# Optimization experiments

Measured on AMD Instinct MI355X. Metric: run time of the kernel, lower is better.

## Reference

```python
import jax, jax.numpy as jnp
import numpy as np

B, N, K, NUM_CLASSES = 8, 4096, 16, 40
M = B * N


def _safe_norm(v):
    s = jnp.sum(v * v, axis=-1)
    return jnp.where(s > 0, jnp.sqrt(jnp.where(s > 0, s, 1.0)), 0.0)


def _angle(v1, v2):
    cn = _safe_norm(jnp.cross(v1, v2))
    d = jnp.sum(v1 * v2, axis=-1)
    ok = (cn > 0) | (d != 0)
    return jnp.where(ok, jnp.arctan2(cn, jnp.where(ok, d, 1.0)), 0.0)


def _ppf(pos_i, pos_j, n_i, n_j):
    # PyG point_pair_features: pseudo = pos_j - pos_i (j = source, i = target)
    pseudo = pos_j - pos_i
    return jnp.stack([_safe_norm(pseudo), _angle(n_i, pseudo),
                      _angle(n_j, pseudo), _angle(n_i, n_j)], axis=-1)


def _knn_edges(pos):
    # knn_graph(k=K, loop=False), per-graph; returns (src, dst) with self-loops
    # appended (PPFConv add_self_loops=True default).
    p = pos.reshape(B, N, 3)
    sq = jnp.sum(p * p, axis=-1)                                   # [B,N]
    d2 = sq[:, :, None] + sq[:, None, :] - 2.0 * jnp.einsum('bnd,bmd->bnm', p, p)
    d2 = jnp.where(jnp.eye(N, dtype=bool)[None], jnp.inf, d2)      # no loops
    _, nbr = jax.lax.top_k(-d2, K)                                  # [B,N,K]
    offs = (jnp.arange(B) * N)[:, None, None]
    src = (nbr + offs).reshape(-1)                                  # neighbors j
    dst = jnp.repeat(jnp.arange(M), K)                              # targets i
    loops = jnp.arange(M)
    return jnp.concatenate([src, loops]), jnp.concatenate([dst, loops])


def _mlp(e, w1, b1, w2, b2):
    return jax.nn.relu(e @ w1 + b1) @ w2 + b2


def setup_inputs() -> dict:
    key = jax.random.key(0)
    ks = jax.random.split(key, 12)
    pos = jax.random.normal(ks[0], (M, 3), jnp.float32)
    nrm = jax.random.normal(ks[1], (M, 3), jnp.float32)
    nrm = nrm / jnp.linalg.norm(nrm, axis=-1, keepdims=True)
    batch = jnp.repeat(jnp.arange(B, dtype=jnp.int32), N)
    s = 0.1
    return {
        'pos': pos, 'normal': nrm, 'batch': batch,
        'w1a': jax.random.normal(ks[2], (4, 32)) * s,  'b1a': jnp.zeros(32),
        'w1b': jax.random.normal(ks[3], (32, 32)) * s, 'b1b': jnp.zeros(32),
        'w2a': jax.random.normal(ks[4], (36, 32)) * s, 'b2a': jnp.zeros(32),
        'w2b': jax.random.normal(ks[5], (32, 32)) * s, 'b2b': jnp.zeros(32),
        'wc':  jax.random.normal(ks[6], (32, NUM_CLASSES)) * s,
        'bc':  jnp.zeros(NUM_CLASSES),
    }


def reference(pos, normal, batch, w1a, b1a, w1b, b1b, w2a, b2a, w2b, b2b, wc, bc):
    src, dst = _knn_edges(pos)
    feats = _ppf(pos[dst], pos[src], normal[dst], normal[src])      # [E,4]
    # conv1: x=None -> message = mlp1(ppf), scatter-max per target node
    msg1 = _mlp(feats, w1a, b1a, w1b, b1b)
    x = jax.nn.relu(jax.ops.segment_max(msg1, dst, num_segments=M))  # [M,32]
    # conv2: message = mlp2([x_j, ppf])
    msg2 = _mlp(jnp.concatenate([x[src], feats], axis=-1), w2a, b2a, w2b, b2b)
    x = jax.nn.relu(jax.ops.segment_max(msg2, dst, num_segments=M))
    # global_max_pool over each graph (uniform batch: reshape)
    g = x.reshape(B, N, 32).max(axis=1)                              # [B,32]
    return g @ wc + bc                                               # [B,40]
```

## Files before the change

kernel.cpp:

```cpp
#include <hip/hip_runtime.h>
#include <hip/hip_bf16.h>
#include <math.h>

#define NB 8
#define NN 4096
#define KK 16
#define MM (NB*NN)
#define CH 32
#define SLOTS 17
#define NCLS 40
#define BIG 3.0e38f
#define CAP 96
#define NPB 32
#define NBLK (MM/NPB)
#define HROW 36
#define HALF 2048

#define OW1A 0
#define OB1A 128
#define OW1B 160
#define OB1B 1184
#define OW2A 1216
#define OB2A 2368
#define OW2B 2400
#define OB2B 3424
#define OWC  3456
#define OBC  4736
#define NWTS 4776

typedef short short8 __attribute__((ext_vector_type(8)));
typedef float f32x4  __attribute__((ext_vector_type(4)));
typedef float f32x2  __attribute__((ext_vector_type(2)));

__device__ float4 g_pos4[MM];
__device__ float4 g_nrm4[MM];
__device__ int    g_nbr[MM*KK];
__device__ float  g_u[MM*CH];
__device__ float  g_bmax[NBLK*CH];
__device__ float  g_wts[NWTS];
__device__ __align__(16) float4 g_fe4[MM*SLOTS];
__device__ __align__(16) unsigned short g_wfrag1[2][2][64][8];
__device__ __align__(16) unsigned short g_wfrag2[2][2][64][8];

__device__ __forceinline__ float bf(const __hip_bfloat16 x) { return __bfloat162float(x); }

__device__ __forceinline__ float ldf(const void* p, int i, bool f32) {
  return f32 ? ((const float*)p)[i] : bf(((const __hip_bfloat16*)p)[i]);
}

__device__ __forceinline__ float angf(float ax, float ay, float az,
                                      float bx, float by, float bz) {
  float cx = ay*bz - az*by;
  float cy = az*bx - ax*bz;
  float cz = ax*by - ay*bx;
  float s  = cx*cx + cy*cy + cz*cz;
  float cn = s > 0.f ? sqrtf(s) : 0.f;
  float d  = ax*bx + ay*by + az*bz;
  return (cn > 0.f || d != 0.f) ? atan2f(cn, d) : 0.f;
}

__device__ __forceinline__ void ppf4(const float4 pi, const float4 ni,
                                     const float4 pj, const float4 nj, float* f) {
  float px = pj.x - pi.x, py = pj.y - pi.y, pz = pj.z - pi.z;
  float s = px*px + py*py + pz*pz;
  f[0] = s > 0.f ? sqrtf(s) : 0.f;
  f[1] = angf(ni.x, ni.y, ni.z, px, py, pz);
  f[2] = angf(nj.x, nj.y, nj.z, px, py, pz);
  f[3] = angf(ni.x, ni.y, ni.z, nj.x, nj.y, nj.z);
}

__device__ __forceinline__ unsigned int fkey(float f) {
  unsigned int u = __float_as_uint(f);
  return (u & 0x80000000u) ? ~u : (u | 0x80000000u);
}
__device__ __forceinline__ float funkey(unsigned int k) {
  unsigned int u = (k & 0x80000000u) ? (k ^ 0x80000000u) : ~k;
  return __uint_as_float(u);
}

__device__ __forceinline__ unsigned int mbcnt64(unsigned long long m) {
  return __builtin_amdgcn_mbcnt_hi((unsigned int)(m >> 32),
         __builtin_amdgcn_mbcnt_lo((unsigned int)m, 0u));
}

__device__ __forceinline__ void bsplit(float v, unsigned short* hi, unsigned short* lo) {
  __hip_bfloat16 h = __float2bfloat16(v);
  float hf = __bfloat162float(h);
  __hip_bfloat16 l = __float2bfloat16(v - hf);
  *hi = *reinterpret_cast<unsigned short*>(&h);
  *lo = *reinterpret_cast<unsigned short*>(&l);
}

__device__ __forceinline__ void afrag(const float* row, short8* ah, short8* al) {
  float4 a = *(const float4*)row;
  float4 b = *(const float4*)(row + 4);
  unsigned short h, l;
  #pragma unroll
  for (int j = 0; j < 4; ++j) {
    bsplit((&a.x)[j], &h, &l); (*ah)[j]   = (short)h; (*al)[j]   = (short)l;
    bsplit((&b.x)[j], &h, &l); (*ah)[j+4] = (short)h; (*al)[j+4] = (short)l;
  }
}

__global__ __launch_bounds__(256) void prep_kernel(
    const void* __restrict__ pos, const void* __restrict__ nrm,
    const void* w1a, const void* b1a, const void* w1b, const void* b1b,
    const void* w2a, const void* b2a, const void* w2b, const void* b2b,
    const void* wc, const void* bc) {
  __shared__ int sflag;
  const int tid = threadIdx.x;
  const int base = blockIdx.x << 8;
  if (tid < 64) {
    const float* nf = (const float*)nrm;
    const __hip_bfloat16* nh = (const __hip_bfloat16*)nrm;
    int n = base + tid;
    float x = nf[3*n], y = nf[3*n+1], z = nf[3*n+2];
    float ss = x*x + y*y + z*z;
    bool okf = (ss > 0.98f && ss < 1.02f);
    float a = bf(nh[3*n]), b2 = bf(nh[3*n+1]), c2 = bf(nh[3*n+2]);
    float sb = a*a + b2*b2 + c2*c2;
    bool okb = (sb > 0.95f && sb < 1.05f);
    unsigned long long mf = __ballot(okf), mb = __ballot(okb);
    if (tid == 0) sflag = (__popcll(mf) >= __popcll(mb)) ? 1 : 0;
  }
  __syncthreads();
  const bool f32 = sflag != 0;
  {
    int i = base + tid;
    float x = ldf(pos, 3*i, f32), y = ldf(pos, 3*i+1, f32), z = ldf(pos, 3*i+2, f32);
    g_pos4[i] = make_float4(x, y, z, x*x + y*y + z*z);
    float a = ldf(nrm, 3*i, f32), bb = ldf(nrm, 3*i+1, f32), cc = ldf(nrm, 3*i+2, f32);
    g_nrm4[i] = make_float4(a, bb, cc, 0.f);
  }
  if (blockIdx.x == 0) {
    for (int t = tid; t < 128;  t += 256) g_wts[OW1A + t] = ldf(w1a, t, f32);
    for (int t = tid; t < 32;   t += 256) g_wts[OB1A + t] = ldf(b1a, t, f32);
    for (int t = tid; t < 1024; t += 256) g_wts[OW1B + t] = ldf(w1b, t, f32);
    for (int t = tid; t < 32;   t += 256) g_wts[OB1B + t] = ldf(b1b, t, f32);
    for (int t = tid; t < 1152; t += 256) g_wts[OW2A + t] = ldf(w2a, t, f32);
    for (int t = tid; t < 32;   t += 256) g_wts[OB2A + t] = ldf(b2a, t, f32);
    for (int t = tid; t < 1024; t += 256) g_wts[OW2B + t] = ldf(w2b, t, f32);
    for (int t = tid; t < 32;   t += 256) g_wts[OB2B + t] = ldf(b2b, t, f32);
    for (int t = tid; t < 1280; t += 256) g_wts[OWC  + t] = ldf(wc,  t, f32);
    for (int t = tid; t < 40;   t += 256) g_wts[OBC  + t] = ldf(bc,  t, f32);
    for (int t = tid; t < 4096; t += 256) {
      int which = t >> 11;
      int r = t & 2047;
      int tt = r >> 10;  r &= 1023;
      int hl = r >> 9;   r &= 511;
      int ln = r >> 3;
      int j  = r & 7;
      int k = (ln >> 4)*8 + j;
      int c = tt*16 + (ln & 15);
      float wv = ldf(which ? w2b : w1b, k*CH + c, f32);
      unsigned short hi, lo;
      bsplit(wv, &hi, &lo);
      unsigned short v = hl ? lo : hi;
      if (which) g_wfrag2[tt][hl][ln][j] = v;
      else       g_wfrag1[tt][hl][ln][j] = v;
    }
  }
}

__global__ __launch_bounds__(512, 8) void knn_conv1_kernel() {
  __shared__ __align__(16) union SU {
    struct {
      float sx[HALF], sy[HALF], sz[HALF];
      unsigned short ilst[NPB][CAP];
      double dlst[8][CAP];
    } k;
    struct {
      float fe[NPB*SLOTS][4];
      float h1s[152*HROW];
      float wsaT[32*HROW];
      float xs[NPB][CH];
    } c;
  } u;
  __shared__ unsigned short nbrs[NPB][KK];

  const int tid  = threadIdx.x;
  const int w    = tid >> 6, lane = tid & 63;
  const int blk  = blockIdx.x;
  const int b    = blk >> 7;
  const int qb   = (blk & 127) << 5;
  const float4* bp = g_pos4 + b*NN;

  float q2x[4], q2y[4], q2z[4];
  #pragma unroll
  for (int qq = 0; qq < 4; ++qq) {
    float4 qv = bp[qb + (w << 2) + qq];
    q2x[qq] = -2.f*qv.x; q2y[qq] = -2.f*qv.y; q2z[qq] = -2.f*qv.z;
  }

  const f32x2* sx2 = (const f32x2*)u.k.sx;
  const f32x2* sy2 = (const f32x2*)u.k.sy;
  const f32x2* sz2 = (const f32x2*)u.k.sz;

  float mn[4];
  #pragma unroll
  for (int qq = 0; qq < 4; ++qq) mn[qq] = BIG;
  #pragma unroll 1
  for (int h = 0; h < 2; ++h) {
    #pragma unroll
    for (int k = 0; k < 4; ++k) {
      int idx = k*512 + tid;
      float4 o = bp[h*HALF + idx];
      u.k.sx[idx] = o.x; u.k.sy[idx] = o.y; u.k.sz[idx] = o.z;
    }
    __syncthreads();
    #pragma unroll 4
    for (int it = 0; it < 16; ++it) {
      int p = it*64 + lane;
      f32x2 ox = sx2[p], oy = sy2[p], oz = sz2[p];
      f32x2 ow = __builtin_elementwise_fma(oz, oz,
                 __builtin_elementwise_fma(oy, oy, ox*ox));
      #pragma unroll
      for (int qq = 0; qq < 4; ++qq) {
        f32x2 qx = {q2x[qq], q2x[qq]};
        f32x2 qy = {q2y[qq], q2y[qq]};
        f32x2 qz = {q2z[qq], q2z[qq]};
        f32x2 d = __builtin_elementwise_fma(qx, ox,
                  __builtin_elementwise_fma(qy, oy,
                  __builtin_elementwise_fma(qz, oz, ow)));
        mn[qq] = fminf(fminf(d[0], d[1]), mn[qq]);
      }
    }
    __syncthreads();
  }

  unsigned int key[4], lo[4], hi[4];
  #pragma unroll
  for (int qq = 0; qq < 4; ++qq) { key[qq] = fkey(mn[qq]) >> 16; lo[qq] = 0u; hi[qq] = 0xFFFFu; }
  #pragma unroll 1
  for (int s = 0; s < 16; ++s) {
    #pragma unroll
    for (int qq = 0; qq < 4; ++qq) {
      unsigned int mid = (lo[qq] + hi[qq]) >> 1;
      int c = (int)__popcll(__ballot(key[qq] <= mid));
      if (c >= 17) hi[qq] = mid; else lo[qq] = mid + 1;
    }
  }
  float Tf[4];
  #pragma unroll
  for (int qq = 0; qq < 4; ++qq) {
    float T = funkey((hi[qq] << 16) | 0xFFFFu);
    Tf[qq] = T + 4e-5f + 1e-5f*fabsf(T);
  }

  unsigned int scnt[4];
  #pragma unroll
  for (int qq = 0; qq < 4; ++qq) scnt[qq] = 0u;
  #pragma unroll 1
  for (int h = 0; h < 2; ++h) {
    #pragma unroll
    for (int k = 0; k < 4; ++k) {
      int idx = k*512 + tid;
      float4 o = bp[h*HALF + idx];
      u.k.sx[idx] = o.x; u.k.sy[idx] = o.y; u.k.sz[idx] = o.z;
    }
    __syncthreads();
    #pragma unroll 2
    for (int it = 0; it < 16; ++it) {
      int p = it*64 + lane;
      int gidx = h*HALF + 2*p;
      f32x2 ox = sx2[p], oy = sy2[p], oz = sz2[p];
      f32x2 ow = __builtin_elementwise_fma(oz, oz,
                 __builtin_elementwise_fma(oy, oy, ox*ox));
      #pragma unroll
      for (int qq = 0; qq < 4; ++qq) {
        f32x2 qx = {q2x[qq], q2x[qq]};
        f32x2 qy = {q2y[qq], q2y[qq]};
        f32x2 qz = {q2z[qq], q2z[qq]};
        f32x2 d = __builtin_elementwise_fma(qx, ox,
                  __builtin_elementwise_fma(qy, oy,
                  __builtin_elementwise_fma(qz, oz, ow)));
        bool h0 = d[0] <= Tf[qq];
        bool h1 = d[1] <= Tf[qq];
        unsigned long long mk0 = __ballot(h0);
        unsigned long long mk1 = __ballot(h1);
        if (mk0 | mk1) {
          unsigned int cbase = scnt[qq];
          if (h0) {
            unsigned int pos = cbase + mbcnt64(mk0);
            if (pos < CAP) u.k.ilst[(w<<2)|qq][pos] = (unsigned short)gidx;
          }
          cbase += (unsigned int)__popcll(mk0);
          if (h1) {
            unsigned int pos = cbase + mbcnt64(mk1);
            if (pos < CAP) u.k.ilst[(w<<2)|qq][pos] = (unsigned short)(gidx + 1);
          }
          scnt[qq] = cbase + (unsigned int)__popcll(mk1);
        }
      }
    }
    __syncthreads();
  }

  #pragma unroll 1
  for (int qq = 0; qq < 4; ++qq) {
    const int ql = (w << 2) | qq;
    const int m = min((int)scnt[qq], CAP);
    const double mx = (double)(-0.5f*q2x[qq]);
    const double my_ = (double)(-0.5f*q2y[qq]);
    const double mz = (double)(-0.5f*q2z[qq]);
    const double sqme = (mx*mx + my_*my_) + mz*mz;
    for (int e = lane; e < m; e += 64) {
      int ci = u.k.ilst[ql][e];
      float4 cv = bp[ci];
      double ox = (double)cv.x, oy = (double)cv.y, oz = (double)cv.z;
      double sqo = (ox*ox + oy*oy) + oz*oz;
      double dt  = (mx*ox + my_*oy) + mz*oz;
      u.k.dlst[w][e] = (sqme + sqo) - 2.0*dt;
    }
    for (int e = lane; e < m; e += 64) {
      double myd = u.k.dlst[w][e];
      int myi = u.k.ilst[ql][e];
      int rank = 0;
      for (int o = 0; o < m; ++o) {
        double od = u.k.dlst[w][o];
        int oi = u.k.ilst[ql][o];
        rank += (od < myd) || (od == myd && oi < myi);
      }
      if (rank >= 1 && rank <= KK) {
        nbrs[ql][rank-1] = (unsigned short)myi;
        g_nbr[(b*NN + qb + ql)*KK + (rank-1)] = b*NN + myi;
      }
    }
  }

  const int c32 = tid & 31;
  const int quad = lane >> 4, l15 = lane & 15;
  float w1a_c[4];
  #pragma unroll
  for (int f = 0; f < 4; ++f) w1a_c[f] = g_wts[OW1A + f*CH + c32];
  const float b1a_c = g_wts[OB1A + c32];
  short8 bH0 = *(const short8*)&g_wfrag1[0][0][lane][0];
  short8 bL0 = *(const short8*)&g_wfrag1[0][1][lane][0];
  short8 bH1 = *(const short8*)&g_wfrag1[1][0][lane][0];
  short8 bL1 = *(const short8*)&g_wfrag1[1][1][lane][0];
  const float bias0 = g_wts[OB1B + l15];
  const float bias1 = g_wts[OB1B + 16 + l15];

  __syncthreads();

  for (int i2 = tid; i2 < 1024; i2 += 512) {
    int k = i2 >> 5, cc = i2 & 31;
    u.c.wsaT[cc*HROW + k] = g_wts[OW2A + i2];
  }
  const int nbb = b*NN + qb;
  for (int e = tid; e < NPB*SLOTS; e += 512) {
    int ns = e / 17, slot = e - ns*17;
    int ig = nbb + ns;
    int jg = (slot < KK) ? (b*NN + (int)nbrs[ns][slot]) : ig;
    float f[4];
    ppf4(g_pos4[ig], g_nrm4[ig], g_pos4[jg], g_nrm4[jg], f);
    float4 fv = make_float4(f[0], f[1], f[2], f[3]);
    *(float4*)u.c.fe[e] = fv;
    g_fe4[(size_t)nbb*SLOTS + e] = fv;
  }
  __syncthreads();

  #pragma unroll 1
  for (int ck = 0; ck < 4; ++ck) {
    #pragma unroll
    for (int it = 0; it < 9; ++it) {
      int idx = it*512 + tid;
      int e = idx >> 5;
      if (e < 136) {
        float4 f4 = *(const float4*)u.c.fe[ck*136 + e];
        float h = b1a_c + f4.x*w1a_c[0] + f4.y*w1a_c[1] + f4.z*w1a_c[2] + f4.w*w1a_c[3];
        u.c.h1s[e*HROW + c32] = fmaxf(h, 0.f);
      }
    }
    __syncthreads();
    {
      const int rbase = w*17;
      short8 ah0, al0, ah1, al1;
      afrag(&u.c.h1s[(rbase      + l15)*HROW + quad*8], &ah0, &al0);
      afrag(&u.c.h1s[(rbase + 16 + l15)*HROW + quad*8], &ah1, &al1);
      f32x4 a00 = {0.f,0.f,0.f,0.f}, a01 = a00, a10 = a00, a11 = a00;
      a00 = __builtin_amdgcn_mfma_f32_16x16x32_bf16(ah0, bH0, a00, 0, 0, 0);
      a00 = __builtin_amdgcn_mfma_f32_16x16x32_bf16(ah0, bL0, a00, 0, 0, 0);
      a00 = __builtin_amdgcn_mfma_f32_16x16x32_bf16(al0, bH0, a00, 0, 0, 0);
      a01 = __builtin_amdgcn_mfma_f32_16x16x32_bf16(ah0, bH1, a01, 0, 0, 0);
      a01 = __builtin_amdgcn_mfma_f32_16x16x32_bf16(ah0, bL1, a01, 0, 0, 0);
      a01 = __builtin_amdgcn_mfma_f32_16x16x32_bf16(al0, bH1, a01, 0, 0, 0);
      a10 = __builtin_amdgcn_mfma_f32_16x16x32_bf16(ah1, bH0, a10, 0, 0, 0);
      a10 = __builtin_amdgcn_mfma_f32_16x16x32_bf16(ah1, bL0, a10, 0, 0, 0);
      a10 = __builtin_amdgcn_mfma_f32_16x16x32_bf16(al1, bH0, a10, 0, 0, 0);
      a11 = __builtin_amdgcn_mfma_f32_16x16x32_bf16(ah1, bH1, a11, 0, 0, 0);
      a11 = __builtin_amdgcn_mfma_f32_16x16x32_bf16(ah1, bL1, a11, 0, 0, 0);
      a11 = __builtin_amdgcn_mfma_f32_16x16x32_bf16(al1, bH1, a11, 0, 0, 0);
      float m0 = fmaxf(fmaxf(a00[0], a00[1]), fmaxf(a00[2], a00[3]));
      float m1 = fmaxf(fmaxf(a01[0], a01[1]), fmaxf(a01[2], a01[3]));
      if (quad == 0) { m0 = fmaxf(m0, a10[0]); m1 = fmaxf(m1, a11[0]); }
      m0 = fmaxf(m0, __shfl_xor(m0, 16)); m0 = fmaxf(m0, __shfl_xor(m0, 32));
      m1 = fmaxf(m1, __shfl_xor(m1, 16)); m1 = fmaxf(m1, __shfl_xor(m1, 32));
      if (quad == 0) {
        u.c.xs[ck*8 + w][l15]      = fmaxf(m0 + bias0, 0.f);
        u.c.xs[ck*8 + w][16 + l15] = fmaxf(m1 + bias1, 0.f);
      }
    }
    __syncthreads();
  }
  #pragma unroll
  for (int it = 0; it < 2; ++it) {
    int ns = it*16 + (tid >> 5);
    float uu = 0.f;
    #pragma unroll
    for (int k4 = 0; k4 < 8; ++k4) {
      float4 x4 = *(const float4*)&u.c.xs[ns][4*k4];
      float4 w4 = *(const float4*)&u.c.wsaT[c32*HROW + 4*k4];
      uu += x4.x*w4.x + x4.y*w4.y + x4.z*w4.z + x4.w*w4.w;
    }
    g_u[(nbb + ns)*CH + c32] = uu;
  }
}

__global__ __launch_bounds__(512, 8) void conv2_kernel() {
  __shared__ __align__(16) float fe[NPB*SLOTS][4];
  __shared__ int jn[NPB*SLOTS];
  __shared__ __align__(16) float h1s[152*HROW];
  __shared__ float xs[NPB][CH];
  const int tid = threadIdx.x;
  const int c = tid & 31;
  const int lane = tid & 63, wv = tid >> 6;
  const int quad = lane >> 4, l15 = lane & 15;
  const int node0 = blockIdx.x << 5;
  float w2aL_c[4];
  #pragma unroll
  for (int f = 0; f < 4; ++f) w2aL_c[f] = g_wts[OW2A + (CH + f)*CH + c];
  const float b2a_c = g_wts[OB2A + c];
  short8 bH0 = *(const short8*)&g_wfrag2[0][0][lane][0];
  short8 bL0 = *(const short8*)&g_wfrag2[0][1][lane][0];
  short8 bH1 = *(const short8*)&g_wfrag2[1][0][lane][0];
  short8 bL1 = *(const short8*)&g_wfrag2[1][1][lane][0];
  const float bias0 = g_wts[OB2B + l15];
  const float bias1 = g_wts[OB2B + 16 + l15];

  for (int e = tid; e < NPB*SLOTS; e += 512) {
    int ns = e / 17, slot = e - ns*17;
    int i = node0 + ns;
    jn[e] = (slot < KK) ? g_nbr[i*KK + slot] : i;
    *(float4*)fe[e] = g_fe4[(size_t)node0*SLOTS + e];
  }
  __syncthreads();

  #pragma unroll 1
  for (int ck = 0; ck < 4; ++ck) {
    #pragma unroll
    for (int it = 0; it < 9; ++it) {
      int idx = it*512 + tid;
      int e = idx >> 5;
      if (e < 136) {
        float4 f4 = *(const float4*)fe[ck*136 + e];
        float uv = g_u[jn[ck*136 + e]*CH + c];
        float h = b2a_c + uv + f4.x*w2aL_c[0] + f4.y*w2aL_c[1] + f4.z*w2aL_c[2] + f4.w*w2aL_c[3];
        h1s[e*HROW + c] = fmaxf(h, 0.f);
      }
    }
    __syncthreads();
    {
      const int rbase = wv*17;
      short8 ah0, al0, ah1, al1;
      afrag(&h1s[(rbase      + l15)*HROW + quad*8], &ah0, &al0);
      afrag(&h1s[(rbase + 16 + l15)*HROW + quad*8], &ah1, &al1);
      f32x4 a00 = {0.f,0.f,0.f,0.f}, a01 = a00, a10 = a00, a11 = a00;
      a00 = __builtin_amdgcn_mfma_f32_16x16x32_bf16(ah0, bH0, a00, 0, 0, 0);
      a00 = __builtin_amdgcn_mfma_f32_16x16x32_bf16(ah0, bL0, a00, 0, 0, 0);
      a00 = __builtin_amdgcn_mfma_f32_16x16x32_bf16(al0, bH0, a00, 0, 0, 0);
      a01 = __builtin_amdgcn_mfma_f32_16x16x32_bf16(ah0, bH1, a01, 0, 0, 0);
      a01 = __builtin_amdgcn_mfma_f32_16x16x32_bf16(ah0, bL1, a01, 0, 0, 0);
      a01 = __builtin_amdgcn_mfma_f32_16x16x32_bf16(al0, bH1, a01, 0, 0, 0);
      a10 = __builtin_amdgcn_mfma_f32_16x16x32_bf16(ah1, bH0, a10, 0, 0, 0);
      a10 = __builtin_amdgcn_mfma_f32_16x16x32_bf16(ah1, bL0, a10, 0, 0, 0);
      a10 = __builtin_amdgcn_mfma_f32_16x16x32_bf16(al1, bH0, a10, 0, 0, 0);
      a11 = __builtin_amdgcn_mfma_f32_16x16x32_bf16(ah1, bH1, a11, 0, 0, 0);
      a11 = __builtin_amdgcn_mfma_f32_16x16x32_bf16(ah1, bL1, a11, 0, 0, 0);
      a11 = __builtin_amdgcn_mfma_f32_16x16x32_bf16(al1, bH1, a11, 0, 0, 0);
      float m0 = fmaxf(fmaxf(a00[0], a00[1]), fmaxf(a00[2], a00[3]));
      float m1 = fmaxf(fmaxf(a01[0], a01[1]), fmaxf(a01[2], a01[3]));
      if (quad == 0) { m0 = fmaxf(m0, a10[0]); m1 = fmaxf(m1, a11[0]); }
      m0 = fmaxf(m0, __shfl_xor(m0, 16)); m0 = fmaxf(m0, __shfl_xor(m0, 32));
      m1 = fmaxf(m1, __shfl_xor(m1, 16)); m1 = fmaxf(m1, __shfl_xor(m1, 32));
      if (quad == 0) {
        xs[ck*8 + wv][l15]      = fmaxf(m0 + bias0, 0.f);
        xs[ck*8 + wv][16 + l15] = fmaxf(m1 + bias1, 0.f);
      }
    }
    __syncthreads();
  }
  if (tid < CH) {
    float m2 = xs[0][c];
    #pragma unroll
    for (int r = 1; r < NPB; ++r) m2 = fmaxf(m2, xs[r][c]);
    g_bmax[blockIdx.x*CH + c] = m2;
  }
}

__global__ __launch_bounds__(256) void head_kernel(float* __restrict__ out) {
  __shared__ float red[8][CH];
  __shared__ float gm[CH];
  const int g = blockIdx.x;
  const int c = threadIdx.x & 31, sub = threadIdx.x >> 5;
  const float* base = g_bmax + (size_t)(g*128 + sub*16)*CH;
  float mx = 0.f;
  #pragma unroll
  for (int n = 0; n < 16; ++n) mx = fmaxf(mx, base[n*CH + c]);
  red[sub][c] = mx;
  __syncthreads();
  if (threadIdx.x < CH) {
    float m2 = red[0][c];
    #pragma unroll
    for (int r = 1; r < 8; ++r) m2 = fmaxf(m2, red[r][c]);
    gm[c] = m2;
  }
  __syncthreads();
  if (threadIdx.x < NCLS) {
    int co = threadIdx.x;
    float s = g_wts[OBC + co];
    #pragma unroll
    for (int f = 0; f < CH; ++f) s += gm[f] * g_wts[OWC + f*NCLS + co];
    out[g*NCLS + co] = s;
  }
}

extern "C" void kernel_launch(void* const* d_in, const int* in_sizes, int n_in,
                              void* d_out, int out_size, void* d_ws, size_t ws_size,
                              hipStream_t stream) {
  const void* pos = d_in[0];
  const void* nrm = d_in[1];
  const void* w1a = d_in[3];
  const void* b1a = d_in[4];
  const void* w1b = d_in[5];
  const void* b1b = d_in[6];
  const void* w2a = d_in[7];
  const void* b2a = d_in[8];
  const void* w2b = d_in[9];
  const void* b2b = d_in[10];
  const void* wc  = d_in[11];
  const void* bc  = d_in[12];

  prep_kernel<<<MM/256, 256, 0, stream>>>(pos, nrm, w1a, b1a, w1b, b1b,
                                          w2a, b2a, w2b, b2b, wc, bc);
  knn_conv1_kernel<<<NBLK, 512, 0, stream>>>();
  conv2_kernel<<<NBLK, 512, 0, stream>>>();
  head_kernel<<<NB, 256, 0, stream>>>((float*)d_out);
}
```

Baseline: 212.2 us.

## Fuse head into conv2 via last-block atomic, reuse resident KNN half

The separate head kernel is folded into conv2: each block bumps a per-graph atomic counter, and the last block of each graph reduces the block maxima and computes the classifier logits, then resets the counter. In the KNN pass, the second scan starts on the half of the point cloud already in shared memory, which saves one reload and a barrier. The launch-bounds min-blocks hint of 8 is also dropped, giving the compiler more room for registers. The fused head relies on a threadfence and atomic for cross-block visibility and adds a tail of serial work in the last block of each graph.

```diff
diff --git a/kernel.cpp b/kernel.cpp
--- a/kernel.cpp
+++ b/kernel.cpp
@@ -38,6 +38,7 @@
 __device__ float  g_u[MM*CH];
 __device__ float  g_bmax[NBLK*CH];
 __device__ float  g_wts[NWTS];
+__device__ int    g_cnt[NB];
 __device__ __align__(16) float4 g_fe4[MM*SLOTS];
 __device__ __align__(16) unsigned short g_wfrag1[2][2][64][8];
 __device__ __align__(16) unsigned short g_wfrag2[2][2][64][8];
@@ -162,7 +163,7 @@
   }
 }
 
-__global__ __launch_bounds__(512, 8) void knn_conv1_kernel() {
+__global__ __launch_bounds__(512) void knn_conv1_kernel() {
   __shared__ __align__(16) union SU {
     struct {
       float sx[HALF], sy[HALF], sz[HALF];
@@ -225,7 +226,7 @@
         mn[qq] = fminf(fminf(d[0], d[1]), mn[qq]);
       }
     }
-    __syncthreads();
+    if (h == 0) __syncthreads();
   }
 
   unsigned int key[4], lo[4], hi[4];
@@ -251,14 +252,18 @@
   #pragma unroll
   for (int qq = 0; qq < 4; ++qq) scnt[qq] = 0u;
   #pragma unroll 1
-  for (int h = 0; h < 2; ++h) {
-    #pragma unroll
-    for (int k = 0; k < 4; ++k) {
-      int idx = k*512 + tid;
-      float4 o = bp[h*HALF + idx];
-      u.k.sx[idx] = o.x; u.k.sy[idx] = o.y; u.k.sz[idx] = o.z;
-    }
-    __syncthreads();
+  for (int hh = 0; hh < 2; ++hh) {
+    const int h = 1 - hh;
+    if (hh == 1) {
+      __syncthreads();
+      #pragma unroll
+      for (int k = 0; k < 4; ++k) {
+        int idx = k*512 + tid;
+        float4 o = bp[h*HALF + idx];
+        u.k.sx[idx] = o.x; u.k.sy[idx] = o.y; u.k.sz[idx] = o.z;
+      }
+      __syncthreads();
+    }
     #pragma unroll 2
     for (int it = 0; it < 16; ++it) {
       int p = it*64 + lane;
@@ -293,7 +298,6 @@
         }
       }
     }
-    __syncthreads();
   }
 
   #pragma unroll 1
@@ -417,11 +421,14 @@
   }
 }
 
-__global__ __launch_bounds__(512, 8) void conv2_kernel() {
+__global__ __launch_bounds__(512) void conv2_kernel(float* __restrict__ out) {
   __shared__ __align__(16) float fe[NPB*SLOTS][4];
   __shared__ int jn[NPB*SLOTS];
   __shared__ __align__(16) float h1s[152*HROW];
   __shared__ float xs[NPB][CH];
+  __shared__ float red2[16][CH];
+  __shared__ float gm2[CH];
+  __shared__ int slast;
   const int tid = threadIdx.x;
   const int c = tid & 31;
   const int lane = tid & 63, wv = tid >> 6;
@@ -496,32 +503,32 @@
     for (int r = 1; r < NPB; ++r) m2 = fmaxf(m2, xs[r][c]);
     g_bmax[blockIdx.x*CH + c] = m2;
   }
-}
-
-__global__ __launch_bounds__(256) void head_kernel(float* __restrict__ out) {
-  __shared__ float red[8][CH];
-  __shared__ float gm[CH];
-  const int g = blockIdx.x;
-  const int c = threadIdx.x & 31, sub = threadIdx.x >> 5;
-  const float* base = g_bmax + (size_t)(g*128 + sub*16)*CH;
-  float mx = 0.f;
-  #pragma unroll
-  for (int n = 0; n < 16; ++n) mx = fmaxf(mx, base[n*CH + c]);
-  red[sub][c] = mx;
+  __threadfence();
+  const int g = blockIdx.x >> 7;
+  if (tid == 0) slast = (atomicAdd(&g_cnt[g], 1) == 127) ? 1 : 0;
   __syncthreads();
-  if (threadIdx.x < CH) {
-    float m2 = red[0][c];
-    #pragma unroll
-    for (int r = 1; r < 8; ++r) m2 = fmaxf(m2, red[r][c]);
-    gm[c] = m2;
-  }
-  __syncthreads();
-  if (threadIdx.x < NCLS) {
-    int co = threadIdx.x;
-    float s = g_wts[OBC + co];
-    #pragma unroll
-    for (int f = 0; f < CH; ++f) s += gm[f] * g_wts[OWC + f*NCLS + co];
-    out[g*NCLS + co] = s;
+  if (slast) {
+    const float* basep = g_bmax + (size_t)(g << 7)*CH;
+    const int grp = tid >> 5;
+    float mx = 0.f;
+    #pragma unroll
+    for (int r = 0; r < 8; ++r) mx = fmaxf(mx, basep[(grp*8 + r)*CH + c]);
+    red2[grp][c] = mx;
+    __syncthreads();
+    if (tid < CH) {
+      float m2 = red2[0][c];
+      #pragma unroll
+      for (int r = 1; r < 16; ++r) m2 = fmaxf(m2, red2[r][c]);
+      gm2[c] = m2;
+    }
+    __syncthreads();
+    if (tid < NCLS) {
+      float s = g_wts[OBC + tid];
+      #pragma unroll
+      for (int f = 0; f < CH; ++f) s += gm2[f] * g_wts[OWC + f*NCLS + tid];
+      out[g*NCLS + tid] = s;
+    }
+    if (tid == 0) g_cnt[g] = 0;
   }
 }
 
@@ -544,6 +551,5 @@
   prep_kernel<<<MM/256, 256, 0, stream>>>(pos, nrm, w1a, b1a, w1b, b1b,
                                           w2a, b2a, w2b, b2b, wc, bc);
   knn_conv1_kernel<<<NBLK, 512, 0, stream>>>();
-  conv2_kernel<<<NBLK, 512, 0, stream>>>();
-  head_kernel<<<NB, 256, 0, stream>>>((float*)d_out);
-}
+  conv2_kernel<<<NBLK, 512, 0, stream>>>((float*)d_out);
+}
```

New measurement: 333.8 us. 57.3% more time.
